# Optimization experiments

Hardware: AMD Instinct MI355X
Metric: run time of the kernel (lower is better)

Reference implementation:

```python
import jax, jax.numpy as jnp
import numpy as np

N_USERS = 50000
N_ITEMS = 40000
D = 64
E = 1_000_000
NB = 3       # behaviors
L = 2        # GCN layers per behavior
B = 8192
N_NODES = (N_USERS + 1) + (N_ITEMS + 1)
REG_WEIGHT = 0.01
CL_TEMP = 0.1
BPR_GAMMA = 1e-10


def setup_inputs() -> dict:
    key = jax.random.key(0)
    k1, k2, k3, k4, k5 = jax.random.split(key, 5)
    user_emb = jax.random.normal(k1, (N_USERS + 1, D), jnp.float32) * 0.1
    item_emb = jax.random.normal(k2, (N_ITEMS + 1, D), jnp.float32) * 0.1
    gcn_w = jax.random.normal(k3, (NB, L, D, D), jnp.float32) * 0.1
    gcn_b = jnp.zeros((NB, L, D), jnp.float32)
    edge_index = jax.random.randint(k4, (NB, 2, E), 0, N_NODES, dtype=jnp.int64)
    batch_data = jax.random.randint(k5, (B, NB, 3), 0, 40000, dtype=jnp.int64)
    return {"user_emb": user_emb, "item_emb": item_emb, "gcn_w": gcn_w,
            "gcn_b": gcn_b, "edge_index": edge_index, "batch_data": batch_data}


def gcn_layer(x, edge_index, W, b):
    # PyG GCNConv(add_self_loops=False): h = x @ W; out[col] += norm * h[row]; out += b
    row, col = edge_index[0], edge_index[1]
    n = x.shape[0]
    deg = jnp.zeros((n,), x.dtype).at[col].add(1.0)
    dinv = jnp.where(deg > 0, jax.lax.rsqrt(jnp.maximum(deg, 1.0)), 0.0)
    norm = dinv[row] * dinv[col]                    # [E]
    h = x @ W                                       # [N, D]
    msg = h[row] * norm[:, None]                    # [E, D] gather
    out = jnp.zeros_like(x).at[col].add(msg)        # scatter-add
    return out + b


def _cos(a, b):
    num = jnp.sum(a * b, axis=-1)
    den = jnp.maximum(jnp.linalg.norm(a, axis=-1) * jnp.linalg.norm(b, axis=-1), 1e-8)
    return num / den


def reference(user_emb, item_emb, gcn_w, gcn_b, edge_index, batch_data):
    total = jnp.concatenate([user_emb, item_emb], axis=0)   # [N_NODES, D]
    total_loss = jnp.float32(0.0)
    te = total
    for bi in range(NB):
        # gcn propagate for this behavior (eval: dropout is identity)
        le = te
        for l in range(L):
            le = gcn_layer(le, edge_index[bi], gcn_w[bi, l], gcn_b[bi, l])
        # F.normalize(dim=-1)
        le = le / jnp.maximum(jnp.linalg.norm(le, axis=-1, keepdims=True), 1e-12)
        te = le + te
        # losses for this behavior
        users = batch_data[:, bi, 0]
        items = batch_data[:, bi, 1:]                        # [B, 2]
        ue = te[:N_USERS + 1]
        ie = te[N_USERS + 1:]
        uf = ue[users]                                       # [B, D]
        itf = ie[items]                                      # [B, 2, D]
        pos, neg = itf[:, 0], itf[:, 1]
        # info-nce (cross-entropy over [pos, neg] cosine sims, label 0)
        logits = jnp.stack([_cos(uf, pos), _cos(uf, neg)], axis=1) / CL_TEMP
        cl_loss = jnp.mean(-jax.nn.log_softmax(logits, axis=-1)[:, 0])
        # BPR loss (weight per behavior = 1.0)
        scores = jnp.sum(uf[:, None, :] * itf, axis=2)       # [B, 2]
        bpr = jnp.mean(-jnp.log(BPR_GAMMA + jax.nn.sigmoid(scores[:, 0] - scores[:, 1])))
        total_loss = total_loss + bpr + cl_loss
    # EmbLoss: sum of L2 norms of the raw embedding tables / last table's rows
    emb_loss = (jnp.linalg.norm(user_emb) + jnp.linalg.norm(item_emb)) / item_emb.shape[0]
    return total_loss + REG_WEIGHT * emb_loss
```

## Files before the change

kernel.cpp:

```cpp
#include <hip/hip_runtime.h>
#include <hip/hip_fp16.h>
#include <math.h>

#define NU 50001
#define NI 40001
#define NNODES 90002
#define DD 64
#define EE 1000000
#define NBB 3
#define LL 2
#define BB 8192
#define STRIDE 40
#define QS 16.0f
#define T4U (NU * 16)
#define T4T (NNODES * 16)
#define NBIN 352
#define NPAD (NBIN * 256)
#define CHUNK 4096
#define NBLK 245
#define CAP 64

__global__ __launch_bounds__(512) void k_scatp(const int* __restrict__ edge,
                                               unsigned* __restrict__ binbufP,
                                               unsigned* __restrict__ Hcnt) {
    __shared__ unsigned posc[NBIN];
    int bi = blockIdx.y, blk = blockIdx.x, tid = threadIdx.x;
    for (int i = tid; i < NBIN; i += 512) posc[i] = 0;
    __syncthreads();
    const int* rowp = edge + (size_t)bi * 2 * EE;
    const int* colp = rowp + EE;
    unsigned* bb = binbufP + (size_t)bi * NBIN * NBLK * CAP;
    int base = blk * CHUNK;
    for (int k = 0; k < CHUNK / 512; k++) {
        int e = base + k * 512 + tid;
        if (e < EE) {
            unsigned c = (unsigned)colp[e];
            unsigned bin = c >> 8;
            unsigned pos = atomicAdd(&posc[bin], 1u);
            if (pos < CAP)
                bb[((size_t)bin * NBLK + blk) * CAP + pos] = ((c & 255u) << 17) | (unsigned)rowp[e];
        }
    }
    __syncthreads();
    for (int i = tid; i < NBIN; i += 512) {
        unsigned v = posc[i];
        Hcnt[((size_t)bi * NBLK + blk) * NBIN + i] = v < CAP ? v : CAP;
    }
}

__global__ __launch_bounds__(256) void k_bucket(const unsigned* __restrict__ Hcnt,
                                                const unsigned* __restrict__ binbufP,
                                                unsigned* __restrict__ cnt3, unsigned* __restrict__ bucket3) {
    __shared__ unsigned lb[256 * STRIDE];
    __shared__ unsigned cl[256];
    __shared__ unsigned so[NBLK + 1];
    int bi = blockIdx.y, bin = blockIdx.x, tid = threadIdx.x;
    cl[tid] = 0;
    if (tid == 0) so[0] = 0;
    if (tid < NBLK) so[tid + 1] = Hcnt[((size_t)bi * NBLK + tid) * NBIN + bin];
    __syncthreads();
    if (tid == 0) {
        unsigned run = 0;
        for (int s = 1; s <= NBLK; s++) { run += so[s]; so[s] = run; }
    }
    __syncthreads();
    unsigned T = so[NBLK];
    const unsigned* bb = binbufP + (size_t)bi * NBIN * NBLK * CAP;
    for (unsigned i = tid; i < T; i += 256) {
        int lo = 0, hi = NBLK;
        while (hi - lo > 1) { int mid = (lo + hi) >> 1; if (so[mid] <= i) lo = mid; else hi = mid; }
        unsigned w = bb[((size_t)bin * NBLK + lo) * CAP + (i - so[lo])];
        unsigned c = w >> 17;
        unsigned pos = atomicAdd(&cl[c], 1u);
        if (pos < STRIDE) lb[c * STRIDE + pos] = w & 0x1FFFFu;
    }
    __syncthreads();
    cnt3[(size_t)bi * NPAD + (size_t)bin * 256 + tid] = cl[tid];
    uint4* dst = (uint4*)(bucket3 + (size_t)bi * NPAD * STRIDE + (size_t)bin * 256 * STRIDE);
    const uint4* srcl = (const uint4*)lb;
    #pragma unroll
    for (int k = 0; k < (256 * STRIDE / 4) / 256; k++)
        dst[k * 256 + tid] = srcl[k * 256 + tid];
}

__global__ __launch_bounds__(256) void k_init(const float* __restrict__ user_emb,
                                              const float* __restrict__ item_emb,
                                              const unsigned* __restrict__ cnt0,
                                              float* __restrict__ te, unsigned* __restrict__ X8a,
                                              float* __restrict__ scal) {
    int i0 = blockIdx.x * 256 + threadIdx.x;
    int stride = gridDim.x * 256;
    float su = 0.f, si = 0.f;
    const float4* u4 = (const float4*)user_emb;
    const float4* i4 = (const float4*)item_emb;
    float4* t4 = (float4*)te;
    for (int i = i0; i < T4T; i += stride) {
        float4 v;
        if (i < T4U) { v = u4[i]; su += v.x * v.x + v.y * v.y + v.z * v.z + v.w * v.w; }
        else         { v = i4[i - T4U]; si += v.x * v.x + v.y * v.y + v.z * v.z + v.w * v.w; }
        t4[i] = v;
        unsigned d = cnt0[i >> 4];
        float q = (d ? rsqrtf((float)d) : 0.f) * QS;
        int p0 = __builtin_amdgcn_cvt_pk_fp8_f32(v.x * q, v.y * q, 0, false);
        p0 = __builtin_amdgcn_cvt_pk_fp8_f32(v.z * q, v.w * q, p0, true);
        X8a[i] = (unsigned)p0;
    }
    #pragma unroll
    for (int o = 32; o > 0; o >>= 1) { su += __shfl_down(su, o); si += __shfl_down(si, o); }
    __shared__ float lsu[4], lsi[4];
    int w = threadIdx.x >> 6;
    if ((threadIdx.x & 63) == 0) { lsu[w] = su; lsi[w] = si; }
    __syncthreads();
    if (threadIdx.x == 0) {
        atomicAdd(scal + 1, lsu[0] + lsu[1] + lsu[2] + lsu[3]);
        atomicAdd(scal + 2, lsi[0] + lsi[1] + lsi[2] + lsi[3]);
    }
}

__global__ __launch_bounds__(256) void k_agg(const unsigned* __restrict__ cnt,
                                             const unsigned* __restrict__ bucket,
                                             const uint2* __restrict__ X8in,
                                             __half* __restrict__ agg) {
    int t = blockIdx.x * 256 + threadIdx.x;
    int r = t >> 6;
    if (r >= NNODES) return;
    int lane = t & 63;
    int j2 = lane & 7;
    int hw = lane >> 3;
    unsigned d = cnt[r];
    unsigned dc = d < STRIDE ? d : STRIDE;
    const unsigned* bk = bucket + (size_t)r * STRIDE;
    unsigned a0 = (hw +  0 < dc) ? bk[hw +  0] : (unsigned)NNODES;
    unsigned a1 = (hw +  8 < dc) ? bk[hw +  8] : (unsigned)NNODES;
    unsigned a2 = (hw + 16 < dc) ? bk[hw + 16] : (unsigned)NNODES;
    unsigned a3 = (hw + 24 < dc) ? bk[hw + 24] : (unsigned)NNODES;
    uint2 w0 = X8in[(size_t)a0 * 8 + j2];
    uint2 w1 = X8in[(size_t)a1 * 8 + j2];
    uint2 w2 = X8in[(size_t)a2 * 8 + j2];
    uint2 w3 = X8in[(size_t)a3 * 8 + j2];
    float4 A = {0.f, 0.f, 0.f, 0.f}, Bv = {0.f, 0.f, 0.f, 0.f};
#define ACC8(W) { \
    A.x  += __builtin_amdgcn_cvt_f32_fp8((int)W.x, 0); \
    A.y  += __builtin_amdgcn_cvt_f32_fp8((int)W.x, 1); \
    A.z  += __builtin_amdgcn_cvt_f32_fp8((int)W.x, 2); \
    A.w  += __builtin_amdgcn_cvt_f32_fp8((int)W.x, 3); \
    Bv.x += __builtin_amdgcn_cvt_f32_fp8((int)W.y, 0); \
    Bv.y += __builtin_amdgcn_cvt_f32_fp8((int)W.y, 1); \
    Bv.z += __builtin_amdgcn_cvt_f32_fp8((int)W.y, 2); \
    Bv.w += __builtin_amdgcn_cvt_f32_fp8((int)W.y, 3); }
    ACC8(w0) ACC8(w1) ACC8(w2) ACC8(w3)
    for (unsigned i = hw + 32; i < dc; i += 8) {
        uint2 w = X8in[(size_t)bk[i] * 8 + j2];
        ACC8(w)
    }
#undef ACC8
    #pragma unroll
    for (int o = 8; o <= 32; o <<= 1) {
        A.x  += __shfl_xor(A.x, o);  A.y  += __shfl_xor(A.y, o);
        A.z  += __shfl_xor(A.z, o);  A.w  += __shfl_xor(A.w, o);
        Bv.x += __shfl_xor(Bv.x, o); Bv.y += __shfl_xor(Bv.y, o);
        Bv.z += __shfl_xor(Bv.z, o); Bv.w += __shfl_xor(Bv.w, o);
    }
    if (hw == 0) {
        union { __half2 h[4]; float4 f; } u;
        u.h[0] = __floats2half2_rn(A.x, A.y);
        u.h[1] = __floats2half2_rn(A.z, A.w);
        u.h[2] = __floats2half2_rn(Bv.x, Bv.y);
        u.h[3] = __floats2half2_rn(Bv.z, Bv.w);
        ((float4*)agg)[(size_t)r * 8 + j2] = u.f;
    }
}

template <int FUSE>
__global__ __launch_bounds__(256) void k_gemmE(const __half* __restrict__ agg, const float* __restrict__ W,
                                               const float* __restrict__ b, const unsigned* __restrict__ cnt,
                                               float* __restrict__ te, unsigned* __restrict__ X8out,
                                               const unsigned* __restrict__ cnt_next) {
    __shared__ float ws[64 * 64];
    __shared__ float xs[16][64];
    int tid = threadIdx.x;
    #pragma unroll
    for (int q = 0; q < 4; q++)
        ((float4*)ws)[tid + q * 256] = ((const float4*)W)[tid + q * 256];
    int r0 = blockIdx.x * 16;
    {
        int rr = r0 + (tid >> 4);
        int cc = (tid & 15) * 4;
        if (rr < NNODES) {
            uint2 u = ((const uint2*)agg)[(size_t)rr * 16 + (tid & 15)];
            union { unsigned u; __half2 h; } c0, c1;
            c0.u = u.x; c1.u = u.y;
            float2 f0 = __half22float2(c0.h);
            float2 f1 = __half22float2(c1.h);
            xs[tid >> 4][cc + 0] = f0.x; xs[tid >> 4][cc + 1] = f0.y;
            xs[tid >> 4][cc + 2] = f1.x; xs[tid >> 4][cc + 3] = f1.y;
        }
    }
    __syncthreads();
    int rloc = tid >> 4;
    int j = tid & 15;
    int d4 = j * 4;
    int row = r0 + rloc;
    if (row >= NNODES) return;
    float4 acc = {0.f, 0.f, 0.f, 0.f};
    #pragma unroll
    for (int k = 0; k < 64; k++) {
        float xv = xs[rloc][k];
        float4 wv = *(const float4*)&ws[k * 64 + d4];
        acc.x += xv * wv.x; acc.y += xv * wv.y;
        acc.z += xv * wv.z; acc.w += xv * wv.w;
    }
    unsigned d = cnt[row];
    float m = (d ? rsqrtf((float)d) : 0.f) * (1.0f / QS);
    float4 bb = ((const float4*)b)[j];
    float vx = acc.x * m + bb.x;
    float vy = acc.y * m + bb.y;
    float vz = acc.z * m + bb.z;
    float vw = acc.w * m + bb.w;
    if (FUSE == 0) {
        unsigned dn = cnt_next[row];
        float q = (dn ? rsqrtf((float)dn) : 0.f) * QS;
        int p0 = __builtin_amdgcn_cvt_pk_fp8_f32(vx * q, vy * q, 0, false);
        p0 = __builtin_amdgcn_cvt_pk_fp8_f32(vz * q, vw * q, p0, true);
        X8out[(size_t)row * 16 + j] = (unsigned)p0;
    } else {
        float s = vx * vx + vy * vy + vz * vz + vw * vw;
        #pragma unroll
        for (int o = 1; o <= 8; o <<= 1) s += __shfl_xor(s, o);
        float scale = 1.f / fmaxf(sqrtf(s), 1e-12f);
        float4* te4 = (float4*)te;
        float4 old = te4[(size_t)row * 16 + j];
        old.x += vx * scale; old.y += vy * scale;
        old.z += vz * scale; old.w += vw * scale;
        te4[(size_t)row * 16 + j] = old;
        if (X8out) {
            unsigned dn = cnt_next[row];
            float q = (dn ? rsqrtf((float)dn) : 0.f) * QS;
            int p0 = __builtin_amdgcn_cvt_pk_fp8_f32(old.x * q, old.y * q, 0, false);
            p0 = __builtin_amdgcn_cvt_pk_fp8_f32(old.z * q, old.w * q, p0, true);
            X8out[(size_t)row * 16 + j] = (unsigned)p0;
        }
    }
}

__global__ __launch_bounds__(256) void k_loss(const float* __restrict__ te, const int* __restrict__ batch,
                                              int bi, float* __restrict__ acc) {
    int t = blockIdx.x * 256 + threadIdx.x;
    int s = t >> 6;
    int lane = t & 63;
    if (s >= BB) return;
    const int* bd = &batch[s * (NBB * 3) + bi * 3];
    int u = bd[0], p = bd[1], n = bd[2];
    float uv = te[(size_t)u * DD + lane];
    float pv = te[(size_t)(NU + p) * DD + lane];
    float nv = te[(size_t)(NU + n) * DD + lane];
    float d_up = uv * pv, d_un = uv * nv;
    float s_u = uv * uv, s_p = pv * pv, s_n = nv * nv;
    for (int o = 32; o > 0; o >>= 1) {
        d_up += __shfl_xor(d_up, o);
        d_un += __shfl_xor(d_un, o);
        s_u  += __shfl_xor(s_u, o);
        s_p  += __shfl_xor(s_p, o);
        s_n  += __shfl_xor(s_n, o);
    }
    __shared__ float part[4];
    if (lane == 0) {
        float cosp = d_up / fmaxf(sqrtf(s_u) * sqrtf(s_p), 1e-8f);
        float cosn = d_un / fmaxf(sqrtf(s_u) * sqrtf(s_n), 1e-8f);
        float cl = log1pf(expf((cosn - cosp) * 10.0f));
        float sig = 1.f / (1.f + expf(-(d_up - d_un)));
        float bpr = -logf(1e-10f + sig);
        part[(threadIdx.x >> 6) & 3] = cl + bpr;
    }
    __syncthreads();
    if (threadIdx.x == 0)
        atomicAdd(acc, (part[0] + part[1] + part[2] + part[3]) * (1.0f / BB));
}

__global__ void k_final(const float* __restrict__ scal, float* __restrict__ out) {
    if (threadIdx.x == 0 && blockIdx.x == 0)
        out[0] = scal[0] + 0.01f * (sqrtf(scal[1]) + sqrtf(scal[2])) / 40001.0f;
}

extern "C" void kernel_launch(void* const* d_in, const int* in_sizes, int n_in,
                              void* d_out, int out_size, void* d_ws, size_t ws_size,
                              hipStream_t stream) {
    const float* user_emb = (const float*)d_in[0];
    const float* item_emb = (const float*)d_in[1];
    const float* gcn_w    = (const float*)d_in[2];
    const float* gcn_b    = (const float*)d_in[3];
    const int*   edge_idx = (const int*)d_in[4];
    const int*   batch    = (const int*)d_in[5];
    float* out = (float*)d_out;

    char* ws = (char*)d_ws;
    size_t off = 0;
    auto alloc = [&](size_t bytes) {
        void* p = ws + off;
        off = (off + bytes + 511) & ~(size_t)511;
        return p;
    };
    float*    te      = (float*)alloc((size_t)NNODES * DD * sizeof(float));
    __half*   agg     = (__half*)alloc((size_t)NNODES * DD * sizeof(__half));
    unsigned* X8a     = (unsigned*)alloc((size_t)(NNODES + 1) * 16 * sizeof(unsigned));
    unsigned* X8b     = (unsigned*)alloc((size_t)(NNODES + 1) * 16 * sizeof(unsigned));
    unsigned* cnt3    = (unsigned*)alloc((size_t)NBB * NPAD * sizeof(unsigned));
    unsigned* bucket3 = (unsigned*)alloc((size_t)NBB * NPAD * STRIDE * sizeof(unsigned));
    unsigned* binbufP = (unsigned*)alloc((size_t)NBB * NBIN * NBLK * CAP * sizeof(unsigned));
    unsigned* Hcnt    = (unsigned*)alloc((size_t)NBB * NBLK * NBIN * sizeof(unsigned));
    float*    scal    = (float*)alloc(64 * sizeof(float));

    hipMemsetAsync(scal, 0, 64 * sizeof(float), stream);
    hipMemsetAsync(X8a + (size_t)NNODES * 16, 0, 64, stream);
    hipMemsetAsync(X8b + (size_t)NNODES * 16, 0, 64, stream);

    k_scatp <<<dim3(NBLK, NBB), 512, 0, stream>>>(edge_idx, binbufP, Hcnt);
    k_bucket<<<dim3(NBIN, NBB), 256, 0, stream>>>(Hcnt, binbufP, cnt3, bucket3);

    k_init<<<1024, 256, 0, stream>>>(user_emb, item_emb, cnt3, te, X8a, scal);

    const int gat_grid  = (NNODES * DD + 255) / 256;
    const int gemm_grid = (NNODES + 15) / 16;

    for (int bi = 0; bi < NBB; bi++) {
        const unsigned* cnt = cnt3 + (size_t)bi * NPAD;
        const unsigned* bucket = bucket3 + (size_t)bi * NPAD * STRIDE;
        const float* W0 = gcn_w + ((size_t)bi * LL + 0) * DD * DD;
        const float* b0 = gcn_b + ((size_t)bi * LL + 0) * DD;
        const float* W1 = gcn_w + ((size_t)bi * LL + 1) * DD * DD;
        const float* b1 = gcn_b + ((size_t)bi * LL + 1) * DD;

        k_agg<<<gat_grid, 256, 0, stream>>>(cnt, bucket, (const uint2*)X8a, agg);
        k_gemmE<0><<<gemm_grid, 256, 0, stream>>>(agg, W0, b0, cnt, nullptr, X8b, cnt);

        k_agg<<<gat_grid, 256, 0, stream>>>(cnt, bucket, (const uint2*)X8b, agg);
        unsigned* x8next = (bi < NBB - 1) ? X8a : nullptr;
        const unsigned* cnt_next = cnt3 + (size_t)((bi + 1) % NBB) * NPAD;
        k_gemmE<1><<<gemm_grid, 256, 0, stream>>>(agg, W1, b1, cnt, te, x8next, cnt_next);

        k_loss<<<(BB * 64) / 256, 256, 0, stream>>>(te, batch, bi, scal);
    }

    k_final<<<1, 64, 0, stream>>>(scal, out);
}
```

Baseline: 503.0 us.

## Compact per-block edge bins with local counting sort instead of fixed-capacity slots

The edge binning pass now counts bins in shared memory, prefix-sums the counts, and writes each block's edges as a contiguous, bin-sorted chunk with per-bin offsets. This replaces the padded NBLK×NBIN×CAP slot buffer, which was sparsely written and could drop edges beyond CAP. The bucket kernel reads from the compact buffer through the offsets and replaces its serial prefix sum with a parallel scan. The cost is two passes of shared atomics per edge and extra scan barriers in both kernels.

```diff
diff --git a/kernel.cpp b/kernel.cpp
--- a/kernel.cpp
+++ b/kernel.cpp
@@ -18,58 +18,97 @@
 #define NPAD (NBIN * 256)
 #define CHUNK 4096
 #define NBLK 245
-#define CAP 64
 
 __global__ __launch_bounds__(512) void k_scatp(const int* __restrict__ edge,
-                                               unsigned* __restrict__ binbufP,
-                                               unsigned* __restrict__ Hcnt) {
+                                               unsigned* __restrict__ binbufC,
+                                               unsigned* __restrict__ Hcnt,
+                                               unsigned* __restrict__ Hoff) {
     __shared__ unsigned posc[NBIN];
+    __shared__ unsigned sc[512];
+    __shared__ unsigned lb[CHUNK];
     int bi = blockIdx.y, blk = blockIdx.x, tid = threadIdx.x;
     for (int i = tid; i < NBIN; i += 512) posc[i] = 0;
     __syncthreads();
     const int* rowp = edge + (size_t)bi * 2 * EE;
     const int* colp = rowp + EE;
-    unsigned* bb = binbufP + (size_t)bi * NBIN * NBLK * CAP;
     int base = blk * CHUNK;
-    for (int k = 0; k < CHUNK / 512; k++) {
+    unsigned pk[8], bn[8];
+    #pragma unroll
+    for (int k = 0; k < 8; k++) {
         int e = base + k * 512 + tid;
         if (e < EE) {
             unsigned c = (unsigned)colp[e];
-            unsigned bin = c >> 8;
-            unsigned pos = atomicAdd(&posc[bin], 1u);
-            if (pos < CAP)
-                bb[((size_t)bin * NBLK + blk) * CAP + pos] = ((c & 255u) << 17) | (unsigned)rowp[e];
+            pk[k] = ((c & 255u) << 17) | (unsigned)rowp[e];
+            bn[k] = c >> 8;
+            atomicAdd(&posc[bn[k]], 1u);
+        } else bn[k] = 0xFFFFFFFFu;
+    }
+    __syncthreads();
+    unsigned v = (tid < NBIN) ? posc[tid] : 0u;
+    sc[tid] = v;
+    __syncthreads();
+    #pragma unroll
+    for (int o = 1; o < 512; o <<= 1) {
+        unsigned u = (tid >= o) ? sc[tid - o] : 0u;
+        __syncthreads();
+        sc[tid] += u;
+        __syncthreads();
+    }
+    if (tid < NBIN) {
+        unsigned excl = sc[tid] - v;
+        Hcnt[((size_t)bi * NBLK + blk) * NBIN + tid] = v;
+        Hoff[((size_t)bi * NBLK + blk) * NBIN + tid] = excl;
+        posc[tid] = excl;
+    }
+    __syncthreads();
+    #pragma unroll
+    for (int k = 0; k < 8; k++) {
+        if (bn[k] != 0xFFFFFFFFu) {
+            unsigned pos = atomicAdd(&posc[bn[k]], 1u);
+            lb[pos] = pk[k];
         }
     }
     __syncthreads();
-    for (int i = tid; i < NBIN; i += 512) {
-        unsigned v = posc[i];
-        Hcnt[((size_t)bi * NBLK + blk) * NBIN + i] = v < CAP ? v : CAP;
-    }
+    uint4* d4 = (uint4*)(binbufC + ((size_t)bi * NBLK + blk) * CHUNK);
+    const uint4* s4 = (const uint4*)lb;
+    #pragma unroll
+    for (int k = 0; k < CHUNK / 4 / 512; k++)
+        d4[k * 512 + tid] = s4[k * 512 + tid];
 }
 
 __global__ __launch_bounds__(256) void k_bucket(const unsigned* __restrict__ Hcnt,
-                                                const unsigned* __restrict__ binbufP,
+                                                const unsigned* __restrict__ Hoff,
+                                                const unsigned* __restrict__ binbufC,
                                                 unsigned* __restrict__ cnt3, unsigned* __restrict__ bucket3) {
     __shared__ unsigned lb[256 * STRIDE];
     __shared__ unsigned cl[256];
     __shared__ unsigned so[NBLK + 1];
+    __shared__ unsigned bo[NBLK];
+    __shared__ unsigned sc[256];
     int bi = blockIdx.y, bin = blockIdx.x, tid = threadIdx.x;
     cl[tid] = 0;
+    unsigned v = 0;
+    if (tid < NBLK) {
+        v = Hcnt[((size_t)bi * NBLK + tid) * NBIN + bin];
+        bo[tid] = Hoff[((size_t)bi * NBLK + tid) * NBIN + bin];
+    }
+    sc[tid] = v;
+    __syncthreads();
+    #pragma unroll
+    for (int o = 1; o < 256; o <<= 1) {
+        unsigned u = (tid >= o) ? sc[tid - o] : 0u;
+        __syncthreads();
+        sc[tid] += u;
+        __syncthreads();
+    }
     if (tid == 0) so[0] = 0;
-    if (tid < NBLK) so[tid + 1] = Hcnt[((size_t)bi * NBLK + tid) * NBIN + bin];
-    __syncthreads();
-    if (tid == 0) {
-        unsigned run = 0;
-        for (int s = 1; s <= NBLK; s++) { run += so[s]; so[s] = run; }
-    }
+    if (tid < NBLK) so[tid + 1] = sc[tid];
     __syncthreads();
     unsigned T = so[NBLK];
-    const unsigned* bb = binbufP + (size_t)bi * NBIN * NBLK * CAP;
     for (unsigned i = tid; i < T; i += 256) {
         int lo = 0, hi = NBLK;
         while (hi - lo > 1) { int mid = (lo + hi) >> 1; if (so[mid] <= i) lo = mid; else hi = mid; }
-        unsigned w = bb[((size_t)bin * NBLK + lo) * CAP + (i - so[lo])];
+        unsigned w = binbufC[((size_t)bi * NBLK + lo) * CHUNK + bo[lo] + (i - so[lo])];
         unsigned c = w >> 17;
         unsigned pos = atomicAdd(&cl[c], 1u);
         if (pos < STRIDE) lb[c * STRIDE + pos] = w & 0x1FFFFu;
@@ -306,16 +345,17 @@
     unsigned* X8b     = (unsigned*)alloc((size_t)(NNODES + 1) * 16 * sizeof(unsigned));
     unsigned* cnt3    = (unsigned*)alloc((size_t)NBB * NPAD * sizeof(unsigned));
     unsigned* bucket3 = (unsigned*)alloc((size_t)NBB * NPAD * STRIDE * sizeof(unsigned));
-    unsigned* binbufP = (unsigned*)alloc((size_t)NBB * NBIN * NBLK * CAP * sizeof(unsigned));
+    unsigned* binbufC = (unsigned*)alloc((size_t)NBB * NBLK * CHUNK * sizeof(unsigned));
     unsigned* Hcnt    = (unsigned*)alloc((size_t)NBB * NBLK * NBIN * sizeof(unsigned));
+    unsigned* Hoff    = (unsigned*)alloc((size_t)NBB * NBLK * NBIN * sizeof(unsigned));
     float*    scal    = (float*)alloc(64 * sizeof(float));
 
     hipMemsetAsync(scal, 0, 64 * sizeof(float), stream);
     hipMemsetAsync(X8a + (size_t)NNODES * 16, 0, 64, stream);
     hipMemsetAsync(X8b + (size_t)NNODES * 16, 0, 64, stream);
 
-    k_scatp <<<dim3(NBLK, NBB), 512, 0, stream>>>(edge_idx, binbufP, Hcnt);
-    k_bucket<<<dim3(NBIN, NBB), 256, 0, stream>>>(Hcnt, binbufP, cnt3, bucket3);
+    k_scatp <<<dim3(NBLK, NBB), 512, 0, stream>>>(edge_idx, binbufC, Hcnt, Hoff);
+    k_bucket<<<dim3(NBIN, NBB), 256, 0, stream>>>(Hcnt, Hoff, binbufC, cnt3, bucket3);
 
     k_init<<<1024, 256, 0, stream>>>(user_emb, item_emb, cnt3, te, X8a, scal);
 
```

Result: faster. 485.4 us (-3.5%).
